# Kernel optimization log

Hardware: AMD Instinct MI355X
Metric: run time of the kernel (lower is better)

Reference implementation:

```python
import jax, jax.numpy as jnp
import numpy as np

QUERY_DIM = 512
KEY_DIM = 512
NUM_HEADS = 16
HEAD_DIM = QUERY_DIM // NUM_HEADS


def setup_inputs() -> dict:
    key = jax.random.key(0)
    ks = jax.random.split(key, 10)
    B, T, S = 4, 2048, 2048
    s_q = 1.0 / np.sqrt(QUERY_DIM)
    s_k = 1.0 / np.sqrt(KEY_DIM)
    return {
        "x": jax.random.normal(ks[0], (B, T, QUERY_DIM), dtype=jnp.float32),
        "context": jax.random.normal(ks[1], (B, S, KEY_DIM), dtype=jnp.float32),
        "Wq": jax.random.normal(ks[2], (QUERY_DIM, QUERY_DIM), dtype=jnp.float32) * s_q,
        "bq": jnp.zeros((QUERY_DIM,), dtype=jnp.float32),
        "Wk": jax.random.normal(ks[3], (KEY_DIM, QUERY_DIM), dtype=jnp.float32) * s_k,
        "bk": jnp.zeros((QUERY_DIM,), dtype=jnp.float32),
        "Wv": jax.random.normal(ks[4], (KEY_DIM, QUERY_DIM), dtype=jnp.float32) * s_k,
        "bv": jnp.zeros((QUERY_DIM,), dtype=jnp.float32),
        "Wo": jax.random.normal(ks[5], (QUERY_DIM, QUERY_DIM), dtype=jnp.float32) * s_q,
        "bo": jnp.zeros((QUERY_DIM,), dtype=jnp.float32),
    }


def reference(x, context, Wq, bq, Wk, bk, Wv, bv, Wo, bo):
    B, T, C = x.shape
    S = context.shape[1]
    H, D = NUM_HEADS, HEAD_DIM
    scale = D ** -0.5
    # projections -> [B, H, T/S, D]
    q = (x @ Wq + bq).reshape(B, T, H, D).transpose(0, 2, 1, 3)
    k = (context @ Wk + bk).reshape(B, S, H, D).transpose(0, 2, 1, 3)
    v = (context @ Wv + bv).reshape(B, S, H, D).transpose(0, 2, 1, 3)
    # explicit attention matrix [B, H, T, S] (faithful to the unfused original)
    attn = jnp.einsum("bhtd,bhsd->bhts", q, k) * scale
    attn = jax.nn.softmax(attn, axis=-1)  # dropout is identity in eval mode
    out = jnp.einsum("bhts,bhsd->bhtd", attn, v)
    out = out.transpose(0, 2, 1, 3).reshape(B, T, C)
    return out @ Wo + bo
```

## Files before the change

kernel.cpp:

```cpp
#include <hip/hip_runtime.h>
#include <hip/hip_bf16.h>
#include <cmath>

typedef __bf16 bf16;
typedef __bf16 bf16x2 __attribute__((ext_vector_type(2)));
typedef __bf16 bf16x4 __attribute__((ext_vector_type(4)));
typedef __bf16 bf16x8 __attribute__((ext_vector_type(8)));
typedef float floatx4 __attribute__((ext_vector_type(4)));
typedef unsigned int uintx2 __attribute__((ext_vector_type(2)));
typedef unsigned int uintx4 __attribute__((ext_vector_type(4)));

#define MFMA_BF16(a, b, c) __builtin_amdgcn_mfma_f32_16x16x32_bf16((a), (b), (c), 0, 0, 0)

#if defined(__has_builtin)
#if __has_builtin(__builtin_amdgcn_global_load_lds)
#define HAVE_GLL 1
#endif
#if __has_builtin(__builtin_amdgcn_cvt_pk_bf16_f32)
#define HAVE_PKCVT 1
#endif
#if __has_builtin(__builtin_amdgcn_permlane32_swap) && __has_builtin(__builtin_amdgcn_permlane16_swap)
#define HAVE_PLSWAP 1
#endif
#endif

__device__ __forceinline__ void stage16(const bf16* g, bf16* ldsbase, int lane) {
#ifdef HAVE_GLL
    __builtin_amdgcn_global_load_lds((const __attribute__((address_space(1))) unsigned int*)g,
                                     (__attribute__((address_space(3))) unsigned int*)ldsbase,
                                     16, 0, 0);
#else
    *(int4*)(ldsbase + lane * 8) = *(const int4*)g;
#endif
}

__device__ __forceinline__ unsigned pk2(float a, float b) {
    bf16x2 t;
#ifdef HAVE_PKCVT
    t = __builtin_amdgcn_cvt_pk_bf16_f32(a, b);
#else
    t[0] = (bf16)a;
    t[1] = (bf16)b;
#endif
    return __builtin_bit_cast(unsigned, t);
}

__device__ __forceinline__ uintx2 p32swap(unsigned x, unsigned y) {
#ifdef HAVE_PLSWAP
    auto r = __builtin_amdgcn_permlane32_swap(x, y, false, false);
    uintx2 o;
    o[0] = r[0];
    o[1] = r[1];
    return o;
#else
    const int lane = threadIdx.x & 63;
    const unsigned px = __shfl(x, lane ^ 32);
    const unsigned py = __shfl(y, lane ^ 32);
    uintx2 o;
    o[0] = (lane & 32) ? py : x;
    o[1] = (lane & 32) ? y : px;
    return o;
#endif
}

__device__ __forceinline__ uintx2 p16swap(unsigned x, unsigned y) {
#ifdef HAVE_PLSWAP
    auto r = __builtin_amdgcn_permlane16_swap(x, y, false, false);
    uintx2 o;
    o[0] = r[0];
    o[1] = r[1];
    return o;
#else
    const int lane = threadIdx.x & 63;
    const unsigned px = __shfl(x, lane ^ 16);
    const unsigned py = __shfl(y, lane ^ 16);
    uintx2 o;
    o[0] = (lane & 16) ? py : x;
    o[1] = (lane & 16) ? y : px;
    return o;
#endif
}

__device__ __forceinline__ int detect_bf16(const void* x) {
    const unsigned short* u = (const unsigned short*)x;
    const int lane = threadIdx.x & 63;
    const unsigned short w0 = u[4 * lane], w1 = u[4 * lane + 2];
    const int e0 = (w0 >> 7) & 0xFF, e1 = (w1 >> 7) & 0xFF;
    const unsigned long long b0 = __ballot(e0 >= 96 && e0 <= 158);
    const unsigned long long b1 = __ballot(e1 >= 96 && e1 <= 158);
    return (__popcll(b0) + __popcll(b1)) >= 90;
}

struct PrepArgs {
    const void* x;
    const void* ctx;
    const void* W[4];
    const void* bias[4];
    bf16* xc;
    bf16* ctxc;
    bf16* WT[4];
    bf16* biasc;
};

__global__ __launch_bounds__(256) void prep(PrepArgs a) {
    const int tid = threadIdx.x;
    const int f = detect_bf16(a.x);
    const int bid = blockIdx.x;
    if (bid < 1024) {
        const int w = bid >> 8, tileid = bid & 255;
        const int bx = tileid & 15, by = tileid >> 4;
        const void* __restrict__ in = a.W[w];
        bf16* __restrict__ out = a.WT[w];
        __shared__ bf16 tile[32][33];
        const int tx = tid & 31, ty = tid >> 5;
        const int x = bx * 32 + tx;
        const int y0 = by * 32;
#pragma unroll
        for (int yy = ty; yy < 32; yy += 8) {
            const size_t idx = (size_t)(y0 + yy) * 512 + x;
            const float v = f ? (float)((const bf16*)in)[idx] : ((const float*)in)[idx];
            tile[yy][tx] = (bf16)v;
        }
        __syncthreads();
        const int xo = by * 32 + tx;
        const int y1 = bx * 32;
#pragma unroll
        for (int yy = ty; yy < 32; yy += 8)
            out[(size_t)(y1 + yy) * 512 + xo] = tile[tx][yy];
    } else if (bid < 5120) {
        if (f) return;
        const int seg = (bid >= 3072);
        const void* src = seg ? a.ctx : a.x;
        bf16* dst = seg ? a.ctxc : a.xc;
        const int off = (bid - (seg ? 3072 : 1024)) * 256 + tid;
        const float4 p = ((const float4*)src)[2 * off];
        const float4 q = ((const float4*)src)[2 * off + 1];
        bf16x8 o;
        o[0] = (bf16)p.x; o[1] = (bf16)p.y; o[2] = (bf16)p.z; o[3] = (bf16)p.w;
        o[4] = (bf16)q.x; o[5] = (bf16)q.y; o[6] = (bf16)q.z; o[7] = (bf16)q.w;
        *(bf16x8*)(dst + (size_t)off * 8) = o;
    } else {
        for (int e = tid; e < 2048; e += 256) {
            const int seg = e >> 9, off = e & 511;
            const float v =
                f ? (float)((const bf16*)a.bias[seg])[off] : ((const float*)a.bias[seg])[off];
            a.biasc[seg * 512 + off] = (bf16)v;
        }
    }
}

struct QkvArgs {
    const void* xraw;
    const void* ctxraw;
    const bf16* Aconv[3];
    const bf16* Wt[3];
    const bf16* bias;
    bf16* out[3];
    float scale[3];
};

__global__ __launch_bounds__(256) void gemm_qkv(QkvArgs a) {
    __shared__ __align__(16) bf16 lA[128 * 32];
    __shared__ __align__(16) bf16 lB[128 * 32];
    const int z = blockIdx.z;
    const int f = detect_bf16(a.xraw);
    const bf16* __restrict__ A =
        f ? (const bf16*)(z == 0 ? a.xraw : a.ctxraw) : a.Aconv[z];
    const bf16* __restrict__ Wt = a.Wt[z];
    const int tid = threadIdx.x, wave = tid >> 6, lane = tid & 63;
    const int qd = lane >> 4, j = lane & 15;
    const int m0 = blockIdx.x * 128, n0 = blockIdx.y * 128;
    const int wrow = (wave & 1) * 64, wcol = (wave >> 1) * 64;
    const int srow = wave * 16 + (lane >> 2);
    const int scol = (lane & 3) * 8;
    const bf16* agp = A + (size_t)(m0 + srow) * 512 + scol;
    const bf16* bgp = Wt + (size_t)(n0 + srow) * 512 + scol;
    bf16* lA0 = lA + wave * 512;
    bf16* lB0 = lB + wave * 512;

    floatx4 acc[4][4] = {};

    for (int k0 = 0; k0 < 512; k0 += 32) {
        stage16(agp + k0, lA0, lane);
        stage16(agp + k0 + (size_t)64 * 512, lA0 + 64 * 32, lane);
        stage16(bgp + k0, lB0, lane);
        stage16(bgp + k0 + (size_t)64 * 512, lB0 + 64 * 32, lane);
        __syncthreads();
        bf16x8 af[4], bfr[4];
#pragma unroll
        for (int i = 0; i < 4; ++i) {
            af[i] = *(const bf16x8*)(lA + (wrow + i * 16 + j) * 32 + qd * 8);
            bfr[i] = *(const bf16x8*)(lB + (wcol + i * 16 + j) * 32 + qd * 8);
        }
        if (z < 2) {
#pragma unroll
            for (int nt = 0; nt < 4; ++nt)
#pragma unroll
                for (int rf = 0; rf < 4; ++rf)
                    acc[nt][rf] = MFMA_BF16(bfr[nt], af[rf], acc[nt][rf]);
        } else {
#pragma unroll
            for (int rf = 0; rf < 4; ++rf)
#pragma unroll
                for (int nt = 0; nt < 4; ++nt)
                    acc[rf][nt] = MFMA_BF16(af[rf], bfr[nt], acc[rf][nt]);
        }
        __syncthreads();
    }

    const float scale = a.scale[z];
    const bf16* bias = a.bias + z * 512;
    bf16* __restrict__ C = a.out[z];
    if (z < 2) {
#pragma unroll
        for (int nt = 0; nt < 4; ++nt) {
            const int nb = n0 + wcol + nt * 16 + qd * 4;
            const bf16x4 bv4 = *(const bf16x4*)(bias + nb);
            const int h = nb >> 5, d0 = nb & 31;
#pragma unroll
            for (int rf = 0; rf < 4; ++rf) {
                const int m = m0 + wrow + rf * 16 + j;
                const int bb = m >> 11, t = m & 2047;
                bf16x4 pk;
#pragma unroll
                for (int r = 0; r < 4; ++r)
                    pk[r] = (bf16)((acc[nt][rf][r] + (float)bv4[r]) * scale);
                *(bf16x4*)(&C[(((size_t)bb * 16 + h) * 2048 + t) * 32 + d0]) = pk;
            }
        }
    } else {
#pragma unroll
        for (int nt = 0; nt < 4; ++nt) {
            const int n = n0 + wcol + nt * 16 + j;
            const float bv = (float)bias[n];
            const int h = n >> 5, d = n & 31;
#pragma unroll
            for (int rf = 0; rf < 4; ++rf) {
                const int t0 = m0 + wrow + rf * 16 + qd * 4;
                const int bb = t0 >> 11, s = t0 & 2047;
                bf16x4 pk;
#pragma unroll
                for (int r = 0; r < 4; ++r) pk[r] = (bf16)(acc[rf][nt][r] + bv);
                *(bf16x4*)(&C[(((size_t)bb * 16 + h) * 32 + d) * 2048 + s]) = pk;
            }
        }
    }
}

__global__ __launch_bounds__(256, 4) void attn_kernel(const bf16* __restrict__ Q,
                                                      const bf16* __restrict__ Kh,
                                                      const bf16* __restrict__ Vt,
                                                      bf16* __restrict__ O) {
    const int tid = threadIdx.x;
    const int wave = tid >> 6, lane = tid & 63;
    const int qd = lane >> 4, j = lane & 15;
    const int bh = blockIdx.x;
    const int b = bh >> 4, h = bh & 15;
    const int tw = blockIdx.y * 128 + wave * 32;

    const bf16* qbase = Q + ((size_t)bh * 2048 + tw) * 32;
    const bf16* kbase = Kh + (size_t)bh * 2048 * 32;
    const bf16* vbase = Vt + (size_t)bh * 32 * 2048;

    bf16x8 qf[2];
#pragma unroll
    for (int tf = 0; tf < 2; ++tf)
        qf[tf] = *(const bf16x8*)(qbase + (size_t)(tf * 16 + j) * 32 + qd * 8);

    bf16x8 ones;
#pragma unroll
    for (int e = 0; e < 8; ++e) ones[e] = (bf16)1.0f;

    const floatx4 zero = {0.f, 0.f, 0.f, 0.f};
    floatx4 oacc[2][2] = {};
    floatx4 dacc[2] = {};

    for (int s0 = 0; s0 < 2048; s0 += 64) {
        bf16x8 kf[4], vf[4];
#pragma unroll
        for (int sf = 0; sf < 4; ++sf)
            kf[sf] = *(const bf16x8*)(kbase + (size_t)(s0 + sf * 16 + j) * 32 + qd * 8);
#pragma unroll
        for (int dt = 0; dt < 2; ++dt)
#pragma unroll
            for (int kk = 0; kk < 2; ++kk)
                vf[dt * 2 + kk] =
                    *(const bf16x8*)(vbase + (size_t)(dt * 16 + j) * 2048 + s0 + kk * 32 + qd * 8);

#pragma unroll
        for (int tf = 0; tf < 2; ++tf) {
            floatx4 sc[4];
#pragma unroll
            for (int sf = 0; sf < 4; ++sf) sc[sf] = MFMA_BF16(kf[sf], qf[tf], zero);
            unsigned SW[4][2];
#pragma unroll
            for (int sf = 0; sf < 4; ++sf) {
                const float e0 = __builtin_amdgcn_exp2f(sc[sf][0]);
                const float e1 = __builtin_amdgcn_exp2f(sc[sf][1]);
                const float e2 = __builtin_amdgcn_exp2f(sc[sf][2]);
                const float e3 = __builtin_amdgcn_exp2f(sc[sf][3]);
                SW[sf][0] = pk2(e0, e1);
                SW[sf][1] = pk2(e2, e3);
            }
            const uintx2 a0 = p32swap(SW[0][0], SW[1][0]);
            const uintx2 a1 = p32swap(SW[0][1], SW[1][1]);
            const uintx2 c0 = p32swap(SW[2][0], SW[3][0]);
            const uintx2 c1 = p32swap(SW[2][1], SW[3][1]);
            const uintx2 t0 = p16swap(a0[0], a0[1]);
            const uintx2 t1 = p16swap(a1[0], a1[1]);
            const uintx2 t2 = p16swap(c0[0], c0[1]);
            const uintx2 t3 = p16swap(c1[0], c1[1]);
            uintx4 w0, w1;
            w0[0] = t0[0]; w0[1] = t1[0]; w0[2] = t0[1]; w0[3] = t1[1];
            w1[0] = t2[0]; w1[1] = t3[0]; w1[2] = t2[1]; w1[3] = t3[1];
            const bf16x8 pf0 = __builtin_bit_cast(bf16x8, w0);
            const bf16x8 pf1 = __builtin_bit_cast(bf16x8, w1);
            oacc[tf][0] = MFMA_BF16(pf0, vf[0], oacc[tf][0]);
            oacc[tf][1] = MFMA_BF16(pf0, vf[2], oacc[tf][1]);
            dacc[tf] = MFMA_BF16(pf0, ones, dacc[tf]);
            oacc[tf][0] = MFMA_BF16(pf1, vf[1], oacc[tf][0]);
            oacc[tf][1] = MFMA_BF16(pf1, vf[3], oacc[tf][1]);
            dacc[tf] = MFMA_BF16(pf1, ones, dacc[tf]);
        }
    }

#pragma unroll
    for (int tf = 0; tf < 2; ++tf)
#pragma unroll
        for (int r = 0; r < 4; ++r) {
            const float inv = 1.0f / dacc[tf][r];
            const int t = tw + tf * 16 + qd * 4 + r;
#pragma unroll
            for (int dt = 0; dt < 2; ++dt)
                O[((size_t)b * 2048 + t) * 512 + h * 32 + dt * 16 + j] =
                    (bf16)(oacc[tf][dt][r] * inv);
        }
}

__global__ __launch_bounds__(256) void gemm_out(const bf16* __restrict__ A,
                                                const bf16* __restrict__ Wt,
                                                const bf16* __restrict__ bias,
                                                void* __restrict__ C,
                                                const void* __restrict__ xraw) {
    __shared__ __align__(16) bf16 lA[128 * 32];
    __shared__ __align__(16) bf16 lB[128 * 32];
    const int oflag = detect_bf16(xraw);
    const int tid = threadIdx.x, wave = tid >> 6, lane = tid & 63;
    const int qd = lane >> 4, j = lane & 15;
    const int m0 = blockIdx.x * 128, n0 = blockIdx.y * 128;
    const int wrow = (wave & 1) * 64, wcol = (wave >> 1) * 64;
    const int srow = wave * 16 + (lane >> 2);
    const int scol = (lane & 3) * 8;
    const bf16* agp = A + (size_t)(m0 + srow) * 512 + scol;
    const bf16* bgp = Wt + (size_t)(n0 + srow) * 512 + scol;
    bf16* lA0 = lA + wave * 512;
    bf16* lB0 = lB + wave * 512;

    floatx4 acc[4][4] = {};

    for (int k0 = 0; k0 < 512; k0 += 32) {
        stage16(agp + k0, lA0, lane);
        stage16(agp + k0 + (size_t)64 * 512, lA0 + 64 * 32, lane);
        stage16(bgp + k0, lB0, lane);
        stage16(bgp + k0 + (size_t)64 * 512, lB0 + 64 * 32, lane);
        __syncthreads();
        bf16x8 af[4], bfr[4];
#pragma unroll
        for (int i = 0; i < 4; ++i) {
            af[i] = *(const bf16x8*)(lA + (wrow + i * 16 + j) * 32 + qd * 8);
            bfr[i] = *(const bf16x8*)(lB + (wcol + i * 16 + j) * 32 + qd * 8);
        }
#pragma unroll
        for (int nt = 0; nt < 4; ++nt)
#pragma unroll
            for (int rf = 0; rf < 4; ++rf)
                acc[nt][rf] = MFMA_BF16(bfr[nt], af[rf], acc[nt][rf]);
        __syncthreads();
    }

#pragma unroll
    for (int nt = 0; nt < 4; ++nt) {
        const int nb = n0 + wcol + nt * 16 + qd * 4;
        const bf16x4 bv4 = *(const bf16x4*)(bias + nb);
#pragma unroll
        for (int rf = 0; rf < 4; ++rf) {
            const int m = m0 + wrow + rf * 16 + j;
            if (oflag) {
                bf16x4 pk;
#pragma unroll
                for (int r = 0; r < 4; ++r) pk[r] = (bf16)(acc[nt][rf][r] + (float)bv4[r]);
                *(bf16x4*)((bf16*)C + (size_t)m * 512 + nb) = pk;
            } else {
                float4 v;
                v.x = acc[nt][rf][0] + (float)bv4[0];
                v.y = acc[nt][rf][1] + (float)bv4[1];
                v.z = acc[nt][rf][2] + (float)bv4[2];
                v.w = acc[nt][rf][3] + (float)bv4[3];
                *(float4*)((float*)C + (size_t)m * 512 + nb) = v;
            }
        }
    }
}

extern "C" void kernel_launch(void* const* d_in, const int* in_sizes, int n_in, void* d_out,
                              int out_size, void* d_ws, size_t ws_size, hipStream_t stream) {
    char* ws = (char*)d_ws;
    bf16* wqT = (bf16*)(ws + 1048576);
    bf16* wkT = (bf16*)(ws + 1572864);
    bf16* wvT = (bf16*)(ws + 2097152);
    bf16* woT = (bf16*)(ws + 2621440);
    bf16* biasc = (bf16*)(ws + 3145728);
    bf16* xc = (bf16*)(ws + 4194304);
    bf16* ctxc = (bf16*)(ws + 12582912);
    bf16* qws = (bf16*)(ws + 20971520);
    bf16* kws = (bf16*)(ws + 29360128);
    bf16* vtws = (bf16*)(ws + 37748736);
    bf16* aws = xc;

    PrepArgs pa;
    pa.x = d_in[0]; pa.ctx = d_in[1];
    pa.W[0] = d_in[2]; pa.W[1] = d_in[4]; pa.W[2] = d_in[6]; pa.W[3] = d_in[8];
    pa.bias[0] = d_in[3]; pa.bias[1] = d_in[5]; pa.bias[2] = d_in[7]; pa.bias[3] = d_in[9];
    pa.xc = xc; pa.ctxc = ctxc;
    pa.WT[0] = wqT; pa.WT[1] = wkT; pa.WT[2] = wvT; pa.WT[3] = woT;
    pa.biasc = biasc;
    prep<<<5121, 256, 0, stream>>>(pa);

    QkvArgs qa;
    qa.xraw = d_in[0]; qa.ctxraw = d_in[1];
    qa.Aconv[0] = xc; qa.Aconv[1] = ctxc; qa.Aconv[2] = ctxc;
    qa.Wt[0] = wqT; qa.Wt[1] = wkT; qa.Wt[2] = wvT;
    qa.bias = biasc;
    qa.out[0] = qws; qa.out[1] = kws; qa.out[2] = vtws;
    qa.scale[0] = 0.2550348593f; qa.scale[1] = 1.0f; qa.scale[2] = 1.0f;
    gemm_qkv<<<dim3(64, 4, 3), 256, 0, stream>>>(qa);

    attn_kernel<<<dim3(64, 16), 256, 0, stream>>>(qws, kws, vtws, aws);

    gemm_out<<<dim3(64, 4), 256, 0, stream>>>(aws, woT, biasc + 3 * 512, d_out, d_in[0]);
}
```

Measured before the change: 230.1 us.

## Software-pipeline attention loop with K/V prefetch and double-buffered P tiles

Restructures the attention inner loop into a two-stage software pipeline. K and V fragments for the next chunk are loaded while the current QK^T/exp work runs, and the PV MFMAs use the probabilities computed in the previous step, kept in two alternating P buffers. Empty asm register pins hold the prefetched fragments in VGPRs, and s_setprio raises wave priority around the PV MFMA burst. The extra live registers lower the launch-bounds occupancy hint from 4 to 3 blocks per CU, giving up some latency hiding across waves in exchange for overlap within each wave.

```diff
diff --git a/kernel.cpp b/kernel.cpp
--- a/kernel.cpp
+++ b/kernel.cpp
@@ -33,6 +33,9 @@
     *(int4*)(ldsbase + lane * 8) = *(const int4*)g;
 #endif
 }
+
+#define PIN4(A)                                                                          \
+    asm volatile("" : "+v"((A)[0]), "+v"((A)[1]), "+v"((A)[2]), "+v"((A)[3]))
 
 __device__ __forceinline__ unsigned pk2(float a, float b) {
     bf16x2 t;
@@ -247,7 +250,7 @@
     }
 }
 
-__global__ __launch_bounds__(256, 4) void attn_kernel(const bf16* __restrict__ Q,
+__global__ __launch_bounds__(256, 3) void attn_kernel(const bf16* __restrict__ Q,
                                                       const bf16* __restrict__ Kh,
                                                       const bf16* __restrict__ Vt,
                                                       bf16* __restrict__ O) {
@@ -275,23 +278,28 @@
     floatx4 oacc[2][2] = {};
     floatx4 dacc[2] = {};
 
-    for (int s0 = 0; s0 < 2048; s0 += 64) {
-        bf16x8 kf[4], vf[4];
+    bf16x8 K[4], Va[4], Vb[4], pfE[4], pfO[4];
+
+    auto loadK = [&](int s0) {
 #pragma unroll
         for (int sf = 0; sf < 4; ++sf)
-            kf[sf] = *(const bf16x8*)(kbase + (size_t)(s0 + sf * 16 + j) * 32 + qd * 8);
+            K[sf] = *(const bf16x8*)(kbase + (size_t)(s0 + sf * 16 + j) * 32 + qd * 8);
+    };
+    auto loadV = [&](int s0, bf16x8* v) {
 #pragma unroll
         for (int dt = 0; dt < 2; ++dt)
 #pragma unroll
             for (int kk = 0; kk < 2; ++kk)
-                vf[dt * 2 + kk] =
+                v[dt * 2 + kk] =
                     *(const bf16x8*)(vbase + (size_t)(dt * 16 + j) * 2048 + s0 + kk * 32 + qd * 8);
-
+    };
+
+    auto qk = [&](bf16x8* pf) {
 #pragma unroll
         for (int tf = 0; tf < 2; ++tf) {
             floatx4 sc[4];
 #pragma unroll
-            for (int sf = 0; sf < 4; ++sf) sc[sf] = MFMA_BF16(kf[sf], qf[tf], zero);
+            for (int sf = 0; sf < 4; ++sf) sc[sf] = MFMA_BF16(K[sf], qf[tf], zero);
             unsigned SW[4][2];
 #pragma unroll
             for (int sf = 0; sf < 4; ++sf) {
@@ -313,16 +321,53 @@
             uintx4 w0, w1;
             w0[0] = t0[0]; w0[1] = t1[0]; w0[2] = t0[1]; w0[3] = t1[1];
             w1[0] = t2[0]; w1[1] = t3[0]; w1[2] = t2[1]; w1[3] = t3[1];
-            const bf16x8 pf0 = __builtin_bit_cast(bf16x8, w0);
-            const bf16x8 pf1 = __builtin_bit_cast(bf16x8, w1);
-            oacc[tf][0] = MFMA_BF16(pf0, vf[0], oacc[tf][0]);
-            oacc[tf][1] = MFMA_BF16(pf0, vf[2], oacc[tf][1]);
-            dacc[tf] = MFMA_BF16(pf0, ones, dacc[tf]);
-            oacc[tf][0] = MFMA_BF16(pf1, vf[1], oacc[tf][0]);
-            oacc[tf][1] = MFMA_BF16(pf1, vf[3], oacc[tf][1]);
-            dacc[tf] = MFMA_BF16(pf1, ones, dacc[tf]);
-        }
-    }
+            pf[tf * 2 + 0] = __builtin_bit_cast(bf16x8, w0);
+            pf[tf * 2 + 1] = __builtin_bit_cast(bf16x8, w1);
+        }
+    };
+    auto pv = [&](const bf16x8* vf, const bf16x8* pf) {
+        __builtin_amdgcn_s_setprio(1);
+#pragma unroll
+        for (int tf = 0; tf < 2; ++tf) {
+            oacc[tf][0] = MFMA_BF16(pf[tf * 2 + 0], vf[0], oacc[tf][0]);
+            oacc[tf][1] = MFMA_BF16(pf[tf * 2 + 0], vf[2], oacc[tf][1]);
+            dacc[tf] = MFMA_BF16(pf[tf * 2 + 0], ones, dacc[tf]);
+            oacc[tf][0] = MFMA_BF16(pf[tf * 2 + 1], vf[1], oacc[tf][0]);
+            oacc[tf][1] = MFMA_BF16(pf[tf * 2 + 1], vf[3], oacc[tf][1]);
+            dacc[tf] = MFMA_BF16(pf[tf * 2 + 1], ones, dacc[tf]);
+        }
+        __builtin_amdgcn_s_setprio(0);
+    };
+
+    loadK(0);
+    loadV(0, Va);
+    qk(pfE);
+    loadK(64);
+    PIN4(Va);
+    PIN4(K);
+
+    int s0 = 0;
+#pragma unroll 1
+    for (int it = 0; it < 15; ++it) {
+        loadV(s0 + 64, Vb);
+        qk(pfO);
+        loadK(s0 + 128);
+        pv(Va, pfE);
+        PIN4(Vb);
+        PIN4(K);
+        loadV(s0 + 128, Va);
+        qk(pfE);
+        loadK(s0 + 192);
+        pv(Vb, pfO);
+        PIN4(Va);
+        PIN4(K);
+        s0 += 128;
+    }
+    loadV(1984, Vb);
+    qk(pfO);
+    pv(Va, pfE);
+    PIN4(Vb);
+    pv(Vb, pfO);
 
 #pragma unroll
     for (int tf = 0; tf < 2; ++tf)
```

After: 248.3 us. 7.9% more time.

## Share K/V tiles across waves via double-buffered LDS with global_load_lds

Applied to the files above, without the earlier changes.

Previously each of the four waves loaded its own K and V fragments from global memory every iteration. Now each wave loads one quarter of the 64-key K/V tile into a double-buffered LDS region with global_load_lds, and all waves read their fragments from LDS. The next tile is prefetched while the current one is computed, with explicit vmcnt waits and workgroup barriers. This cuts redundant global/L2 traffic by four and overlaps loads with MFMA work, at the cost of 16KB of LDS per block and two barriers per iteration, which may lower occupancy.

```diff
diff --git a/kernel.cpp b/kernel.cpp
--- a/kernel.cpp
+++ b/kernel.cpp
@@ -247,6 +247,16 @@
     }
 }
 
+__device__ __forceinline__ void gll16kv(const bf16* g, bf16* lds) {
+#ifdef HAVE_GLL
+    __builtin_amdgcn_global_load_lds((const __attribute__((address_space(1))) unsigned int*)g,
+                                     (__attribute__((address_space(3))) unsigned int*)lds,
+                                     16, 0, 0);
+#else
+    *(int4*)(lds + (threadIdx.x & 63) * 8) = *(const int4*)g;
+#endif
+}
+
 __global__ __launch_bounds__(256, 4) void attn_kernel(const bf16* __restrict__ Q,
                                                       const bf16* __restrict__ Kh,
                                                       const bf16* __restrict__ Vt,
@@ -258,6 +268,9 @@
     const int b = bh >> 4, h = bh & 15;
     const int tw = blockIdx.y * 128 + wave * 32;
 
+    __shared__ __align__(16) bf16 lsK[2][2048];
+    __shared__ __align__(16) bf16 lsV[2][2048];
+
     const bf16* qbase = Q + ((size_t)bh * 2048 + tw) * 32;
     const bf16* kbase = Kh + (size_t)bh * 2048 * 32;
     const bf16* vbase = Vt + (size_t)bh * 32 * 2048;
@@ -267,6 +280,17 @@
     for (int tf = 0; tf < 2; ++tf)
         qf[tf] = *(const bf16x8*)(qbase + (size_t)(tf * 16 + j) * 32 + qd * 8);
 
+    const bf16* ksrc = kbase + (size_t)(wave * 16 + j) * 32 + qd * 8;
+    const bf16* vsrc =
+        vbase + (size_t)((wave >> 1) * 16 + j) * 2048 + (wave & 1) * 32 + qd * 8;
+    bf16* kdst = &lsK[0][wave * 512];
+    bf16* vdst = &lsV[0][wave * 512];
+
+    auto stage = [&](int buf, int s0) {
+        gll16kv(ksrc + (size_t)s0 * 32, kdst + buf * 2048);
+        gll16kv(vsrc + s0, vdst + buf * 2048);
+    };
+
     bf16x8 ones;
 #pragma unroll
     for (int e = 0; e < 8; ++e) ones[e] = (bf16)1.0f;
@@ -275,18 +299,7 @@
     floatx4 oacc[2][2] = {};
     floatx4 dacc[2] = {};
 
-    for (int s0 = 0; s0 < 2048; s0 += 64) {
-        bf16x8 kf[4], vf[4];
-#pragma unroll
-        for (int sf = 0; sf < 4; ++sf)
-            kf[sf] = *(const bf16x8*)(kbase + (size_t)(s0 + sf * 16 + j) * 32 + qd * 8);
-#pragma unroll
-        for (int dt = 0; dt < 2; ++dt)
-#pragma unroll
-            for (int kk = 0; kk < 2; ++kk)
-                vf[dt * 2 + kk] =
-                    *(const bf16x8*)(vbase + (size_t)(dt * 16 + j) * 2048 + s0 + kk * 32 + qd * 8);
-
+    auto qk = [&](const bf16x8* kf, bf16x8* pf) {
 #pragma unroll
         for (int tf = 0; tf < 2; ++tf) {
             floatx4 sc[4];
@@ -313,15 +326,51 @@
             uintx4 w0, w1;
             w0[0] = t0[0]; w0[1] = t1[0]; w0[2] = t0[1]; w0[3] = t1[1];
             w1[0] = t2[0]; w1[1] = t3[0]; w1[2] = t2[1]; w1[3] = t3[1];
-            const bf16x8 pf0 = __builtin_bit_cast(bf16x8, w0);
-            const bf16x8 pf1 = __builtin_bit_cast(bf16x8, w1);
-            oacc[tf][0] = MFMA_BF16(pf0, vf[0], oacc[tf][0]);
-            oacc[tf][1] = MFMA_BF16(pf0, vf[2], oacc[tf][1]);
-            dacc[tf] = MFMA_BF16(pf0, ones, dacc[tf]);
-            oacc[tf][0] = MFMA_BF16(pf1, vf[1], oacc[tf][0]);
-            oacc[tf][1] = MFMA_BF16(pf1, vf[3], oacc[tf][1]);
-            dacc[tf] = MFMA_BF16(pf1, ones, dacc[tf]);
-        }
+            pf[tf * 2 + 0] = __builtin_bit_cast(bf16x8, w0);
+            pf[tf * 2 + 1] = __builtin_bit_cast(bf16x8, w1);
+        }
+    };
+    auto pv = [&](const bf16x8* vf, const bf16x8* pf) {
+#pragma unroll
+        for (int tf = 0; tf < 2; ++tf) {
+            oacc[tf][0] = MFMA_BF16(pf[tf * 2 + 0], vf[0], oacc[tf][0]);
+            oacc[tf][1] = MFMA_BF16(pf[tf * 2 + 0], vf[2], oacc[tf][1]);
+            dacc[tf] = MFMA_BF16(pf[tf * 2 + 0], ones, dacc[tf]);
+            oacc[tf][0] = MFMA_BF16(pf[tf * 2 + 1], vf[1], oacc[tf][0]);
+            oacc[tf][1] = MFMA_BF16(pf[tf * 2 + 1], vf[3], oacc[tf][1]);
+            dacc[tf] = MFMA_BF16(pf[tf * 2 + 1], ones, dacc[tf]);
+        }
+    };
+
+    stage(0, 0);
+
+    int cur = 0;
+#pragma unroll 1
+    for (int c = 0; c < 32; ++c) {
+        if (c < 31) {
+            stage(cur ^ 1, (c + 1) * 64);
+            asm volatile("s_waitcnt vmcnt(2)" ::: "memory");
+        } else {
+            asm volatile("s_waitcnt vmcnt(0)" ::: "memory");
+        }
+        __builtin_amdgcn_sched_barrier(0);
+        __builtin_amdgcn_s_barrier();
+        __builtin_amdgcn_sched_barrier(0);
+
+        bf16x8 kf[4], vf[4], pf[4];
+#pragma unroll
+        for (int sf = 0; sf < 4; ++sf)
+            kf[sf] = *(const bf16x8*)(&lsK[cur][sf * 512 + lane * 8]);
+#pragma unroll
+        for (int i = 0; i < 4; ++i)
+            vf[i] = *(const bf16x8*)(&lsV[cur][i * 512 + lane * 8]);
+        qk(kf, pf);
+        pv(vf, pf);
+
+        __builtin_amdgcn_sched_barrier(0);
+        __builtin_amdgcn_s_barrier();
+        __builtin_amdgcn_sched_barrier(0);
+        cur ^= 1;
     }
 
 #pragma unroll
```

New measurement: 199.5 us. -13.3%, faster.
